# Kernel optimization log

Measured on AMD Instinct MI355X. Metric: run time of the kernel, lower is better.

Reference implementation:

```python
import jax, jax.numpy as jnp
import numpy as np

B, N, DIN, D, HID, C, K = 16, 1024, 768, 512, 128, 20, 64
H = W = 32
EPS = 1e-5  # BatchNorm eps (inference mode with running stats)


def _conv(x, w, pad=0, dil=1):
    return jax.lax.conv_general_dilated(
        x, w, (1, 1), [(pad, pad), (pad, pad)],
        rhs_dilation=(dil, dil),
        dimension_numbers=('NCHW', 'OIHW', 'NCHW'))


def _bn(x, g, b, m, v):
    inv = jax.lax.rsqrt(v + EPS)
    return (x - m[None, :, None, None]) * (g * inv)[None, :, None, None] + b[None, :, None, None]


def _l2norm(x):
    n = jnp.sqrt(jnp.sum(x * x, axis=-1, keepdims=True))
    return x / jnp.maximum(n, 1e-12)  # matches F.normalize(eps=1e-12)


def setup_inputs():
    key = jax.random.key(0)
    ks = jax.random.split(key, 12)

    def conv_w(k, o, i, kh, kw):
        return jax.random.normal(k, (o, i, kh, kw), jnp.float32) / np.sqrt(i * kh * kw)

    def bn_p(k, c):
        k1, k2 = jax.random.split(k)
        return (jnp.ones(c, jnp.float32), jnp.zeros(c, jnp.float32),
                0.1 * jax.random.normal(k1, (c,), jnp.float32),
                jax.random.uniform(k2, (c,), jnp.float32, 0.5, 1.5))

    g0, b0, m0, v0 = bn_p(ks[3], D)
    gr, br, mr, vr = bn_p(ks[4], HID)
    gl, bl, ml, vl = bn_p(ks[5], HID)
    gg, bg, mg, vg = bn_p(ks[6], HID)
    gp, bp, mp, vp = bn_p(ks[7], D)
    return {
        'patch_feats': jax.random.normal(ks[0], (B, N, DIN), jnp.float32),
        'protos': _l2norm(jax.random.normal(ks[1], (C, K, D), jnp.float32)),  # hybrid protos, L2-normed as in __init__
        'w0': conv_w(ks[2], D, DIN, 1, 1), 'g0': g0, 'b0': b0, 'm0': m0, 'v0': v0,
        'wr': conv_w(ks[8], HID, D, 1, 1), 'gr': gr, 'br': br, 'mr': mr, 'vr': vr,
        'wl': conv_w(ks[9], HID, HID, 3, 3), 'gl': gl, 'bl': bl, 'ml': ml, 'vl': vl,
        'wg': conv_w(ks[10], HID, HID, 3, 3), 'gg': gg, 'bg': bg, 'mg': mg, 'vg': vg,
        'wp': conv_w(ks[11], D, 2 * HID, 1, 1), 'gp': gp, 'bp': bp, 'mp': mp, 'vp': vp,
        'wf': conv_w(jax.random.fold_in(key, 99), D, D, 1, 1),
        'bf': jnp.zeros(D, jnp.float32),
        'logit_scale': jnp.float32(10.0),
    }


def reference(patch_feats, protos, w0, g0, b0, m0, v0, wr, gr, br, mr, vr,
              wl, gl, bl, ml, vl, wg, gg, bg, mg, vg, wp, gp, bp, mp, vp,
              wf, bf, logit_scale):
    Bq, Nq, Din = patch_feats.shape
    x = patch_feats.transpose(0, 2, 1).reshape(Bq, Din, H, W)
    # adapter: 1x1 conv -> BN -> ReLU
    x = jax.nn.relu(_bn(_conv(x, w0), g0, b0, m0, v0))
    # ResidualContextBlock
    res = x
    o = jax.nn.relu(_bn(_conv(x, wr), gr, br, mr, vr))
    l = jax.nn.relu(_bn(_conv(o, wl, pad=1), gl, bl, ml, vl))
    g = jax.nn.relu(_bn(_conv(o, wg, pad=2, dil=2), gg, bg, mg, vg))
    o = _bn(_conv(jnp.concatenate([l, g], axis=1), wp), gp, bp, mp, vp)
    x = jax.nn.relu(o + res)
    # final 1x1 conv (with bias)
    x = _conv(x, wf) + bf[None, :, None, None]
    # back to [B, N, D], L2 normalize
    x = x.reshape(Bq, D, Nq).transpose(0, 2, 1)
    x = _l2norm(x)
    # per-class cosine sims + double max reduction (vectorized over classes)
    sims = jnp.einsum('bnd,ckd->bcnk', x, protos)  # [B,C,N,K]
    A = sims.max(axis=-1)                          # [B,C,N] patch->proto max
    act_maps = A.reshape(Bq, C, H, W)
    logits = A.max(axis=-1) * logit_scale          # [B,C]
    return logits, act_maps, x
```

## Files before the change

### kernel.cpp

```cpp
#include <hip/hip_runtime.h>
#include <math.h>

#define BN_EPS 1e-5f

typedef __attribute__((ext_vector_type(8))) short short8v;
typedef __attribute__((ext_vector_type(8))) unsigned short ushort8v;
typedef __attribute__((ext_vector_type(4))) float f32x4;

__device__ __forceinline__ unsigned short f2b(float f) {
    unsigned int u = __float_as_uint(f);
    return (unsigned short)((u + 0x7FFFu + ((u >> 16) & 1u)) >> 16);
}
__device__ __forceinline__ float b2f(unsigned short h) {
    return __uint_as_float(((unsigned int)h) << 16);
}

typedef __attribute__((address_space(1))) const unsigned int gas_uint;
typedef __attribute__((address_space(3))) unsigned int las_uint;
__device__ __forceinline__ void gload16(const void* g, void* l) {
    __builtin_amdgcn_global_load_lds((gas_uint*)g, (las_uint*)l, 16, 0, 0);
}

__global__ __launch_bounds__(256) void f2b_kernel(
    const float* __restrict__ in, unsigned short* __restrict__ out, int n8)
{
    int i = blockIdx.x * 256 + threadIdx.x;
    if (i >= n8) return;
    const float4* p = (const float4*)(in + (size_t)i * 8);
    float4 a = p[0], b = p[1];
    ushort8v r;
    r[0] = f2b(a.x); r[1] = f2b(a.y); r[2] = f2b(a.z); r[3] = f2b(a.w);
    r[4] = f2b(b.x); r[5] = f2b(b.y); r[6] = f2b(b.z); r[7] = f2b(b.w);
    *(ushort8v*)(out + (size_t)i * 8) = r;
}

__global__ __launch_bounds__(256) void f2b_multi(
    const float* __restrict__ w0, const float* __restrict__ wr,
    const float* __restrict__ wp, const float* __restrict__ wf,
    const float* __restrict__ prot,
    unsigned short* __restrict__ w0o, unsigned short* __restrict__ wro,
    unsigned short* __restrict__ wpo, unsigned short* __restrict__ wfo,
    unsigned short* __restrict__ proto)
{
    int i = blockIdx.x * 256 + threadIdx.x;
    const float* src; unsigned short* dst; int off;
    if      (i <  49152) { src = w0;   dst = w0o;   off = i; }
    else if (i <  57344) { src = wr;   dst = wro;   off = i - 49152; }
    else if (i <  73728) { src = wp;   dst = wpo;   off = i - 57344; }
    else if (i < 106496) { src = wf;   dst = wfo;   off = i - 73728; }
    else if (i < 188416) { src = prot; dst = proto; off = i - 106496; }
    else return;
    const float4* p = (const float4*)(src + (size_t)off * 8);
    float4 a = p[0], b = p[1];
    ushort8v r;
    r[0] = f2b(a.x); r[1] = f2b(a.y); r[2] = f2b(a.z); r[3] = f2b(a.w);
    r[4] = f2b(b.x); r[5] = f2b(b.y); r[6] = f2b(b.z); r[7] = f2b(b.w);
    *(ushort8v*)(dst + (size_t)off * 8) = r;
}

__global__ __launch_bounds__(256) void convw_kernel(
    const float* __restrict__ wl, const float* __restrict__ wg,
    unsigned short* __restrict__ out)
{
    int i = blockIdx.x * 256 + threadIdx.x;
    if (i >= 294912) return;
    int br = i >= 147456;
    int j  = i - br * 147456;
    int tap = j >> 14, oc = (j >> 7) & 127, ic = j & 127;
    const float* src = br ? wg : wl;
    out[i] = f2b(src[((oc << 7) + ic) * 9 + tap]);
}

__global__ __launch_bounds__(256) void zero_kernel(unsigned short* __restrict__ p, int n8)
{
    int i = blockIdx.x * 256 + threadIdx.x;
    if (i >= n8) return;
    ushort8v z;
#pragma unroll
    for (int k = 0; k < 8; ++k) z[k] = 0;
    *(ushort8v*)(p + (size_t)i * 8) = z;
}

template <int EPI>
__global__ __launch_bounds__(256, 3) void mfma_gemm(
    const unsigned short* __restrict__ A, int lda,
    const unsigned short* __restrict__ Wt, int ldw,
    void* __restrict__ outp, int ldc, int Kdim,
    const float* __restrict__ bng, const float* __restrict__ bnb,
    const float* __restrict__ bnm, const float* __restrict__ bnv,
    const unsigned short* __restrict__ res, int ldres,
    const float* __restrict__ bias)
{
    __shared__ short8v Asta[2][512];
    __shared__ short8v Bsta[2][512];
    const int t  = threadIdx.x;
    const int l  = t & 63, wv = t >> 6;
    const int wm = wv >> 1, wn = wv & 1;
    const int m0 = blockIdx.x << 7, n0 = blockIdx.y << 7;

    const int r0  = t & 127;
    const int kb0 = t >> 7;

    const unsigned short* Ap = A  + (size_t)(m0 + r0) * lda + kb0 * 8;
    const unsigned short* Bp = Wt + (size_t)(n0 + r0) * ldw + kb0 * 8;

    f32x4 acc[4][4];
#pragma unroll
    for (int mf = 0; mf < 4; ++mf)
#pragma unroll
        for (int nf = 0; nf < 4; ++nf)
#pragma unroll
            for (int j = 0; j < 4; ++j) acc[mf][nf][j] = 0.f;

    const int arow = wm * 64 + (l & 15);
    const int brow = wn * 64 + (l & 15);
    const int kq   = l >> 4;

    const int nK = Kdim >> 5;

#define STAGE_G(buf, k0)                                     \
    do {                                                     \
        gload16(Ap + (k0),      &Asta[buf][wv * 64]);        \
        gload16(Ap + (k0) + 16, &Asta[buf][wv * 64 + 256]);  \
        gload16(Bp + (k0),      &Bsta[buf][wv * 64]);        \
        gload16(Bp + (k0) + 16, &Bsta[buf][wv * 64 + 256]);  \
    } while (0)

    STAGE_G(0, 0);
    __syncthreads();
    int cur = 0;
    for (int ks = 0; ks < nK; ++ks) {
        short8v af[4], bfv[4];
#pragma unroll
        for (int mf = 0; mf < 4; ++mf) af[mf]  = Asta[cur][kq * 128 + arow + mf * 16];
#pragma unroll
        for (int nf = 0; nf < 4; ++nf) bfv[nf] = Bsta[cur][kq * 128 + brow + nf * 16];
        if (ks + 1 < nK) STAGE_G(cur ^ 1, (ks + 1) << 5);
#pragma unroll
        for (int mf = 0; mf < 4; ++mf)
#pragma unroll
            for (int nf = 0; nf < 4; ++nf)
                acc[mf][nf] = __builtin_amdgcn_mfma_f32_16x16x32_bf16(
                    af[mf], bfv[nf], acc[mf][nf], 0, 0, 0);
        __syncthreads();
        cur ^= 1;
    }
#undef STAGE_G

    float s[4], sh[4];
    int cols[4];
#pragma unroll
    for (int nf = 0; nf < 4; ++nf) {
        int col = n0 + wn * 64 + nf * 16 + (l & 15);
        cols[nf] = col;
        if (EPI == 2) { s[nf] = 1.f; sh[nf] = bias[col]; }
        else {
            float sc = bng[col] * rsqrtf(bnv[col] + BN_EPS);
            s[nf]  = sc;
            sh[nf] = bnb[col] - bnm[col] * sc;
        }
    }
#pragma unroll
    for (int mf = 0; mf < 4; ++mf) {
#pragma unroll
        for (int j = 0; j < 4; ++j) {
            int row = m0 + wm * 64 + mf * 16 + kq * 4 + j;
#pragma unroll
            for (int nf = 0; nf < 4; ++nf) {
                float v = acc[mf][nf][j] * s[nf] + sh[nf];
                if (EPI == 1) v += b2f(res[(size_t)row * ldres + cols[nf]]);
                if (EPI != 2) v = fmaxf(v, 0.f);
                if (EPI == 2) {
                    ((float*)outp)[(size_t)row * ldc + cols[nf]] = v;
                } else if (EPI == 3) {
                    int b = row >> 10, h = (row >> 5) & 31, ww = row & 31;
                    size_t pidx = ((size_t)(b * 36 + h + 2) * 36 + (ww + 2)) * 128 + cols[nf];
                    ((unsigned short*)outp)[pidx] = f2b(v);
                } else {
                    ((unsigned short*)outp)[(size_t)row * ldc + cols[nf]] = f2b(v);
                }
            }
        }
    }
}

__global__ __launch_bounds__(256, 3) void conv_mfma(
    const unsigned short* __restrict__ opad,
    const unsigned short* __restrict__ wt_all,
    const float* __restrict__ g1, const float* __restrict__ b1,
    const float* __restrict__ m1, const float* __restrict__ v1,
    const float* __restrict__ g2, const float* __restrict__ b2,
    const float* __restrict__ m2, const float* __restrict__ v2,
    unsigned short* __restrict__ lg)
{
    __shared__ short8v Asta[2][512];
    __shared__ short8v Bsta[2][1024];
    const int t = threadIdx.x;
    const int l = t & 63, wv = t >> 6;
    const int wm = wv >> 1, wn = wv & 1;
    const int m0 = blockIdx.x << 6;
    const int br = blockIdx.y;
    const int dil = 1 + br;
    const unsigned short* wtb = wt_all + (size_t)br * 147456;

    const int r0 = t & 63;
    const int m  = m0 + r0;
    const int bb = m >> 10, h = (m >> 5) & 31, wc = m & 31;
    const ptrdiff_t pbase = ((ptrdiff_t)(bb * 36 + h + 2) * 36 + (wc + 2)) * 128;
    const unsigned short* ApT = opad + pbase + (t >> 6) * 8;
    const unsigned short* BpT = wtb + (size_t)(t & 127) * 128 + (t >> 7) * 8;

    f32x4 acc[2][4];
#pragma unroll
    for (int mf = 0; mf < 2; ++mf)
#pragma unroll
        for (int nf = 0; nf < 4; ++nf)
#pragma unroll
            for (int j = 0; j < 4; ++j) acc[mf][nf][j] = 0.f;

    const int arow = wm * 32 + (l & 15);
    const int bcol = wn * 64 + (l & 15);
    const int kq   = l >> 4;

#define STAGE_C(buf, s)                                                        \
    do {                                                                       \
        int tap_ = (s) >> 1, hh_ = ((s) & 1) * 64;                             \
        int dh_ = tap_ / 3 - 1, dw_ = tap_ % 3 - 1;                            \
        const unsigned short* Ap_ = ApT + (ptrdiff_t)((dh_ * 36 + dw_) * dil) * 128 + hh_; \
        const unsigned short* Bp_ = BpT + (size_t)tap_ * 16384 + hh_;          \
        gload16(Ap_,      &Asta[buf][wv * 64]);                                \
        gload16(Ap_ + 32, &Asta[buf][wv * 64 + 256]);                          \
        gload16(Bp_,      &Bsta[buf][wv * 64]);                                \
        gload16(Bp_ + 16, &Bsta[buf][wv * 64 + 256]);                          \
        gload16(Bp_ + 32, &Bsta[buf][wv * 64 + 512]);                          \
        gload16(Bp_ + 48, &Bsta[buf][wv * 64 + 768]);                          \
    } while (0)

    STAGE_C(0, 0);
    __syncthreads();
    int cur = 0;
    for (int s = 0; s < 18; ++s) {
        short8v af[2][2], bfv[2][4];
#pragma unroll
        for (int kk = 0; kk < 2; ++kk) {
            int kb = kk * 4 + kq;
            af[kk][0] = Asta[cur][kb * 64 + arow];
            af[kk][1] = Asta[cur][kb * 64 + arow + 16];
#pragma unroll
            for (int nf = 0; nf < 4; ++nf)
                bfv[kk][nf] = Bsta[cur][kb * 128 + bcol + nf * 16];
        }
        if (s + 1 < 18) STAGE_C(cur ^ 1, s + 1);
#pragma unroll
        for (int kk = 0; kk < 2; ++kk)
#pragma unroll
            for (int mf = 0; mf < 2; ++mf)
#pragma unroll
                for (int nf = 0; nf < 4; ++nf)
                    acc[mf][nf] = __builtin_amdgcn_mfma_f32_16x16x32_bf16(
                        af[kk][mf], bfv[kk][nf], acc[mf][nf], 0, 0, 0);
        __syncthreads();
        cur ^= 1;
    }
#undef STAGE_C

    const float* gg = br ? g2 : g1;
    const float* gb = br ? b2 : b1;
    const float* gm = br ? m2 : m1;
    const float* gv = br ? v2 : v1;
    float s4[4], sh[4];
    int cols[4];
#pragma unroll
    for (int nf = 0; nf < 4; ++nf) {
        int col = bcol + nf * 16;
        cols[nf] = col;
        float sc = gg[col] * rsqrtf(gv[col] + BN_EPS);
        s4[nf] = sc;
        sh[nf] = gb[col] - gm[col] * sc;
    }
#pragma unroll
    for (int mf = 0; mf < 2; ++mf) {
#pragma unroll
        for (int j = 0; j < 4; ++j) {
            int row = m0 + wm * 32 + mf * 16 + kq * 4 + j;
#pragma unroll
            for (int nf = 0; nf < 4; ++nf) {
                float v = fmaxf(acc[mf][nf][j] * s4[nf] + sh[nf], 0.f);
                lg[(size_t)row * 256 + br * 128 + cols[nf]] = f2b(v);
            }
        }
    }
}

__global__ __launch_bounds__(256) void l2norm_rows(
    float* __restrict__ x, unsigned short* __restrict__ xn)
{
    const int t    = threadIdx.x;
    const int wv   = t >> 6, lane = t & 63;
    const int row  = (blockIdx.x << 2) + wv;
    float* p = x + (size_t)row * 512 + (lane << 3);
    float4 a = *(float4*)p;
    float4 b = *(float4*)(p + 4);
    float ss = a.x * a.x + a.y * a.y + a.z * a.z + a.w * a.w +
               b.x * b.x + b.y * b.y + b.z * b.z + b.w * b.w;
#pragma unroll
    for (int off = 32; off >= 1; off >>= 1) ss += __shfl_xor(ss, off);
    float sc = 1.f / fmaxf(sqrtf(ss), 1e-12f);
    a.x *= sc; a.y *= sc; a.z *= sc; a.w *= sc;
    b.x *= sc; b.y *= sc; b.z *= sc; b.w *= sc;
    *(float4*)p       = a;
    *(float4*)(p + 4) = b;
    ushort8v r;
    r[0] = f2b(a.x); r[1] = f2b(a.y); r[2] = f2b(a.z); r[3] = f2b(a.w);
    r[4] = f2b(b.x); r[5] = f2b(b.y); r[6] = f2b(b.z); r[7] = f2b(b.w);
    *(ushort8v*)(xn + (size_t)row * 512 + (lane << 3)) = r;
}

__global__ __launch_bounds__(256, 3) void sims_mfma(
    const unsigned short* __restrict__ xn,
    const unsigned short* __restrict__ protos,
    float* __restrict__ act)
{
    __shared__ short8v Asta[2][512];
    __shared__ short8v Bsta[2][512];
    const int t = threadIdx.x;
    const int l = t & 63, wv = t >> 6;
    const int wm = wv >> 1, wn = wv & 1;
    const int m0 = blockIdx.x << 7;

    const int r0  = t & 127, kb0 = t >> 7;
    const unsigned short* Ap = xn + (size_t)(m0 + r0) * 512 + kb0 * 8;
    const unsigned short* Bp = protos + ((size_t)blockIdx.y * 128 + r0) * 512 + kb0 * 8;

    f32x4 acc[4][4];
#pragma unroll
    for (int mf = 0; mf < 4; ++mf)
#pragma unroll
        for (int nf = 0; nf < 4; ++nf)
#pragma unroll
            for (int j = 0; j < 4; ++j) acc[mf][nf][j] = 0.f;

    const int arow = wm * 64 + (l & 15);
    const int brow = wn * 64 + (l & 15);
    const int kq   = l >> 4;

#define STAGE_S(buf, k0)                                     \
    do {                                                     \
        gload16(Ap + (k0),      &Asta[buf][wv * 64]);        \
        gload16(Ap + (k0) + 16, &Asta[buf][wv * 64 + 256]);  \
        gload16(Bp + (k0),      &Bsta[buf][wv * 64]);        \
        gload16(Bp + (k0) + 16, &Bsta[buf][wv * 64 + 256]);  \
    } while (0)

    STAGE_S(0, 0);
    __syncthreads();
    int cur = 0;
    for (int ks = 0; ks < 16; ++ks) {
        short8v af[4], bfv[4];
#pragma unroll
        for (int mf = 0; mf < 4; ++mf) af[mf]  = Asta[cur][kq * 128 + arow + mf * 16];
#pragma unroll
        for (int nf = 0; nf < 4; ++nf) bfv[nf] = Bsta[cur][kq * 128 + brow + nf * 16];
        if (ks + 1 < 16) STAGE_S(cur ^ 1, (ks + 1) << 5);
#pragma unroll
        for (int mf = 0; mf < 4; ++mf)
#pragma unroll
            for (int nf = 0; nf < 4; ++nf)
                acc[mf][nf] = __builtin_amdgcn_mfma_f32_16x16x32_bf16(
                    af[mf], bfv[nf], acc[mf][nf], 0, 0, 0);
        __syncthreads();
        cur ^= 1;
    }
#undef STAGE_S

    const int c = (blockIdx.y << 1) + wn;
#pragma unroll
    for (int mf = 0; mf < 4; ++mf) {
        float vj[4];
#pragma unroll
        for (int j = 0; j < 4; ++j) {
            float v = fmaxf(fmaxf(acc[mf][0][j], acc[mf][1][j]),
                            fmaxf(acc[mf][2][j], acc[mf][3][j]));
            v = fmaxf(v, __shfl_xor(v, 1));
            v = fmaxf(v, __shfl_xor(v, 2));
            v = fmaxf(v, __shfl_xor(v, 4));
            v = fmaxf(v, __shfl_xor(v, 8));
            vj[j] = v;
        }
        if ((l & 15) == 0) {
            int rowb = m0 + wm * 64 + mf * 16 + kq * 4;
#pragma unroll
            for (int j = 0; j < 4; ++j) {
                int row = rowb + j;
                int bb = row >> 10, n = row & 1023;
                act[(((size_t)(bb * 20 + c)) << 10) + n] = vj[j];
            }
        }
    }
}

__global__ __launch_bounds__(256) void logits_max(
    const float* __restrict__ act, const float* __restrict__ lsc,
    float* __restrict__ logits)
{
    const int bc = blockIdx.x;
    const int t  = threadIdx.x;
    float4 v = *(const float4*)(act + ((size_t)bc << 10) + (t << 2));
    float mx = fmaxf(fmaxf(v.x, v.y), fmaxf(v.z, v.w));
#pragma unroll
    for (int off = 32; off >= 1; off >>= 1) mx = fmaxf(mx, __shfl_xor(mx, off));
    __shared__ float wmred[4];
    if ((t & 63) == 0) wmred[t >> 6] = mx;
    __syncthreads();
    if (t == 0) {
        float m2 = fmaxf(fmaxf(wmred[0], wmred[1]), fmaxf(wmred[2], wmred[3]));
        logits[bc] = m2 * lsc[0];
    }
}

extern "C" void kernel_launch(void* const* d_in, const int* in_sizes, int n_in,
                              void* d_out, int out_size, void* d_ws, size_t ws_size,
                              hipStream_t stream)
{
    const float* pf   = (const float*)d_in[0];
    const float* prot = (const float*)d_in[1];
    const float* w0   = (const float*)d_in[2];
    const float* g0   = (const float*)d_in[3];
    const float* b0   = (const float*)d_in[4];
    const float* m0v  = (const float*)d_in[5];
    const float* v0   = (const float*)d_in[6];
    const float* wr   = (const float*)d_in[7];
    const float* gr   = (const float*)d_in[8];
    const float* br   = (const float*)d_in[9];
    const float* mr   = (const float*)d_in[10];
    const float* vr   = (const float*)d_in[11];
    const float* wl   = (const float*)d_in[12];
    const float* gl   = (const float*)d_in[13];
    const float* bl   = (const float*)d_in[14];
    const float* ml   = (const float*)d_in[15];
    const float* vl   = (const float*)d_in[16];
    const float* wg   = (const float*)d_in[17];
    const float* gG   = (const float*)d_in[18];
    const float* bG   = (const float*)d_in[19];
    const float* mG   = (const float*)d_in[20];
    const float* vG   = (const float*)d_in[21];
    const float* wp   = (const float*)d_in[22];
    const float* gp   = (const float*)d_in[23];
    const float* bp   = (const float*)d_in[24];
    const float* mp   = (const float*)d_in[25];
    const float* vp   = (const float*)d_in[26];
    const float* wf   = (const float*)d_in[27];
    const float* bf_  = (const float*)d_in[28];
    const float* lsc  = (const float*)d_in[29];

    char* ws = (char*)d_ws;
    unsigned short* pf_bf    = (unsigned short*)(ws);
    unsigned short* w0_bf    = (unsigned short*)(ws + 25165824);
    unsigned short* wr_bf    = (unsigned short*)(ws + 25952256);
    unsigned short* wt_bf    = (unsigned short*)(ws + 26083328);
    unsigned short* wp_bf    = (unsigned short*)(ws + 26673152);
    unsigned short* wf_bf    = (unsigned short*)(ws + 26935296);
    unsigned short* prot_bf  = (unsigned short*)(ws + 27459584);
    unsigned short* x1_bf    = (unsigned short*)(ws + 28770304);
    unsigned short* opad     = (unsigned short*)(ws + 45547520);
    unsigned short* lg_bf    = (unsigned short*)(ws + 50855936);
    unsigned short* x2_bf    = (unsigned short*)(ws + 59244544);
    unsigned short* xn_bf    = (unsigned short*)(ws + 76021760);

    float* out    = (float*)d_out;
    float* logits = out;
    float* act    = out + 320;
    float* xo     = out + 328000;

    f2b_kernel<<<6144, 256, 0, stream>>>(pf, pf_bf, 1572864);
    f2b_multi<<<736, 256, 0, stream>>>(w0, wr, wp, wf, prot,
                                       w0_bf, wr_bf, wp_bf, wf_bf, prot_bf);
    convw_kernel<<<1152, 256, 0, stream>>>(wl, wg, wt_bf);
    zero_kernel<<<1296, 256, 0, stream>>>(opad, 331776);

    mfma_gemm<0><<<dim3(128, 4), 256, 0, stream>>>(
        pf_bf, 768, w0_bf, 768, x1_bf, 512, 768,
        g0, b0, m0v, v0, nullptr, 0, nullptr);

    mfma_gemm<3><<<dim3(128, 1), 256, 0, stream>>>(
        x1_bf, 512, wr_bf, 512, opad, 0, 512,
        gr, br, mr, vr, nullptr, 0, nullptr);

    conv_mfma<<<dim3(256, 2), 256, 0, stream>>>(
        opad, wt_bf, gl, bl, ml, vl, gG, bG, mG, vG, lg_bf);

    mfma_gemm<1><<<dim3(128, 4), 256, 0, stream>>>(
        lg_bf, 256, wp_bf, 256, x2_bf, 512, 256,
        gp, bp, mp, vp, x1_bf, 512, nullptr);

    mfma_gemm<2><<<dim3(128, 4), 256, 0, stream>>>(
        x2_bf, 512, wf_bf, 512, xo, 512, 512,
        nullptr, nullptr, nullptr, nullptr, nullptr, 0, bf_);

    l2norm_rows<<<4096, 256, 0, stream>>>(xo, xn_bf);

    sims_mfma<<<dim3(128, 10), 256, 0, stream>>>(xn_bf, prot_bf, act);

    logits_max<<<320, 256, 0, stream>>>(act, lsc, logits);
}
```

Measured before the change: 198.0 us.

## Deepen K-tile to 64, issue prefetch before LDS reads, add explicit waits and setprio

The GEMM and sims kernels now stage a 64-wide K slice per iteration instead of 32, doubling LDS buffers and halving the number of barrier round-trips. In all three MFMA loops the next-stage global-to-LDS prefetch is issued before the LDS fragment reads. __syncthreads is replaced by explicit vmcnt/lgkmcnt waits, a sched barrier and s_barrier, and s_setprio raises wave priority around the MFMA block. The intent is to hide global latency and cut sync overhead. The larger LDS footprint (64 KB per block) may reduce occupancy under the 3-block launch bound.

Result: slower. 209.5 us (+5.8%).

```diff
diff --git a/kernel.cpp b/kernel.cpp
--- a/kernel.cpp
+++ b/kernel.cpp
@@ -20,6 +20,11 @@
 __device__ __forceinline__ void gload16(const void* g, void* l) {
     __builtin_amdgcn_global_load_lds((gas_uint*)g, (las_uint*)l, 16, 0, 0);
 }
+
+#define VMCNT0()  asm volatile("s_waitcnt vmcnt(0)"  ::: "memory")
+#define LGKM0()   asm volatile("s_waitcnt lgkmcnt(0)" ::: "memory")
+#define SBAR()    __builtin_amdgcn_s_barrier()
+#define SCHED0()  __builtin_amdgcn_sched_barrier(0)
 
 __global__ __launch_bounds__(256) void f2b_kernel(
     const float* __restrict__ in, unsigned short* __restrict__ out, int n8)
@@ -91,18 +96,15 @@
     const unsigned short* __restrict__ res, int ldres,
     const float* __restrict__ bias)
 {
-    __shared__ short8v Asta[2][512];
-    __shared__ short8v Bsta[2][512];
+    __shared__ short8v Asta[2][1024];
+    __shared__ short8v Bsta[2][1024];
     const int t  = threadIdx.x;
     const int l  = t & 63, wv = t >> 6;
     const int wm = wv >> 1, wn = wv & 1;
     const int m0 = blockIdx.x << 7, n0 = blockIdx.y << 7;
 
-    const int r0  = t & 127;
-    const int kb0 = t >> 7;
-
-    const unsigned short* Ap = A  + (size_t)(m0 + r0) * lda + kb0 * 8;
-    const unsigned short* Bp = Wt + (size_t)(n0 + r0) * ldw + kb0 * 8;
+    const unsigned short* Ap = A  + (size_t)(m0 + (t & 127)) * lda + (t >> 7) * 8;
+    const unsigned short* Bp = Wt + (size_t)(n0 + (t & 127)) * ldw + (t >> 7) * 8;
 
     f32x4 acc[4][4];
 #pragma unroll
@@ -115,34 +117,43 @@
     const int arow = wm * 64 + (l & 15);
     const int brow = wn * 64 + (l & 15);
     const int kq   = l >> 4;
-
-    const int nK = Kdim >> 5;
-
-#define STAGE_G(buf, k0)                                     \
-    do {                                                     \
-        gload16(Ap + (k0),      &Asta[buf][wv * 64]);        \
-        gload16(Ap + (k0) + 16, &Asta[buf][wv * 64 + 256]);  \
-        gload16(Bp + (k0),      &Bsta[buf][wv * 64]);        \
-        gload16(Bp + (k0) + 16, &Bsta[buf][wv * 64 + 256]);  \
+    const int nK   = Kdim >> 6;
+
+#define STAGE_G(buf, k0)                                                   \
+    do {                                                                   \
+        _Pragma("unroll")                                                  \
+        for (int i_ = 0; i_ < 4; ++i_) {                                   \
+            gload16(Ap + (k0) + 16 * i_, &Asta[buf][wv * 64 + 256 * i_]);  \
+            gload16(Bp + (k0) + 16 * i_, &Bsta[buf][wv * 64 + 256 * i_]);  \
+        }                                                                  \
     } while (0)
 
     STAGE_G(0, 0);
-    __syncthreads();
+    VMCNT0(); SBAR();
     int cur = 0;
     for (int ks = 0; ks < nK; ++ks) {
-        short8v af[4], bfv[4];
-#pragma unroll
-        for (int mf = 0; mf < 4; ++mf) af[mf]  = Asta[cur][kq * 128 + arow + mf * 16];
-#pragma unroll
-        for (int nf = 0; nf < 4; ++nf) bfv[nf] = Bsta[cur][kq * 128 + brow + nf * 16];
-        if (ks + 1 < nK) STAGE_G(cur ^ 1, (ks + 1) << 5);
-#pragma unroll
-        for (int mf = 0; mf < 4; ++mf)
-#pragma unroll
-            for (int nf = 0; nf < 4; ++nf)
-                acc[mf][nf] = __builtin_amdgcn_mfma_f32_16x16x32_bf16(
-                    af[mf], bfv[nf], acc[mf][nf], 0, 0, 0);
-        __syncthreads();
+        if (ks + 1 < nK) STAGE_G(cur ^ 1, (ks + 1) << 6);
+        short8v af[2][4], bfv[2][4];
+#pragma unroll
+        for (int kk = 0; kk < 2; ++kk) {
+            int kb = kq + 4 * kk;
+#pragma unroll
+            for (int mf = 0; mf < 4; ++mf) af[kk][mf]  = Asta[cur][kb * 128 + arow + mf * 16];
+#pragma unroll
+            for (int nf = 0; nf < 4; ++nf) bfv[kk][nf] = Bsta[cur][kb * 128 + brow + nf * 16];
+        }
+        LGKM0(); SCHED0();
+        __builtin_amdgcn_s_setprio(1);
+#pragma unroll
+        for (int kk = 0; kk < 2; ++kk)
+#pragma unroll
+            for (int mf = 0; mf < 4; ++mf)
+#pragma unroll
+                for (int nf = 0; nf < 4; ++nf)
+                    acc[mf][nf] = __builtin_amdgcn_mfma_f32_16x16x32_bf16(
+                        af[kk][mf], bfv[kk][nf], acc[mf][nf], 0, 0, 0);
+        __builtin_amdgcn_s_setprio(0);
+        VMCNT0(); SBAR();
         cur ^= 1;
     }
 #undef STAGE_G
@@ -237,9 +248,10 @@
     } while (0)
 
     STAGE_C(0, 0);
-    __syncthreads();
+    VMCNT0(); SBAR();
     int cur = 0;
     for (int s = 0; s < 18; ++s) {
+        if (s + 1 < 18) STAGE_C(cur ^ 1, s + 1);
         short8v af[2][2], bfv[2][4];
 #pragma unroll
         for (int kk = 0; kk < 2; ++kk) {
@@ -250,7 +262,8 @@
             for (int nf = 0; nf < 4; ++nf)
                 bfv[kk][nf] = Bsta[cur][kb * 128 + bcol + nf * 16];
         }
-        if (s + 1 < 18) STAGE_C(cur ^ 1, s + 1);
+        LGKM0(); SCHED0();
+        __builtin_amdgcn_s_setprio(1);
 #pragma unroll
         for (int kk = 0; kk < 2; ++kk)
 #pragma unroll
@@ -259,7 +272,8 @@
                 for (int nf = 0; nf < 4; ++nf)
                     acc[mf][nf] = __builtin_amdgcn_mfma_f32_16x16x32_bf16(
                         af[kk][mf], bfv[kk][nf], acc[mf][nf], 0, 0, 0);
-        __syncthreads();
+        __builtin_amdgcn_s_setprio(0);
+        VMCNT0(); SBAR();
         cur ^= 1;
     }
 #undef STAGE_C
@@ -321,16 +335,16 @@
     const unsigned short* __restrict__ protos,
     float* __restrict__ act)
 {
-    __shared__ short8v Asta[2][512];
-    __shared__ short8v Bsta[2][512];
+    __shared__ short8v Asta[2][1024];
+    __shared__ short8v Bsta[2][1024];
     const int t = threadIdx.x;
     const int l = t & 63, wv = t >> 6;
     const int wm = wv >> 1, wn = wv & 1;
     const int m0 = blockIdx.x << 7;
 
-    const int r0  = t & 127, kb0 = t >> 7;
-    const unsigned short* Ap = xn + (size_t)(m0 + r0) * 512 + kb0 * 8;
-    const unsigned short* Bp = protos + ((size_t)blockIdx.y * 128 + r0) * 512 + kb0 * 8;
+    const unsigned short* Ap = xn + (size_t)(m0 + (t & 127)) * 512 + (t >> 7) * 8;
+    const unsigned short* Bp = protos +
+        ((size_t)blockIdx.y * 128 + (t & 127)) * 512 + (t >> 7) * 8;
 
     f32x4 acc[4][4];
 #pragma unroll
@@ -344,31 +358,41 @@
     const int brow = wn * 64 + (l & 15);
     const int kq   = l >> 4;
 
-#define STAGE_S(buf, k0)                                     \
-    do {                                                     \
-        gload16(Ap + (k0),      &Asta[buf][wv * 64]);        \
-        gload16(Ap + (k0) + 16, &Asta[buf][wv * 64 + 256]);  \
-        gload16(Bp + (k0),      &Bsta[buf][wv * 64]);        \
-        gload16(Bp + (k0) + 16, &Bsta[buf][wv * 64 + 256]);  \
+#define STAGE_S(buf, k0)                                                   \
+    do {                                                                   \
+        _Pragma("unroll")                                                  \
+        for (int i_ = 0; i_ < 4; ++i_) {                                   \
+            gload16(Ap + (k0) + 16 * i_, &Asta[buf][wv * 64 + 256 * i_]);  \
+            gload16(Bp + (k0) + 16 * i_, &Bsta[buf][wv * 64 + 256 * i_]);  \
+        }                                                                  \
     } while (0)
 
     STAGE_S(0, 0);
-    __syncthreads();
+    VMCNT0(); SBAR();
     int cur = 0;
-    for (int ks = 0; ks < 16; ++ks) {
-        short8v af[4], bfv[4];
-#pragma unroll
-        for (int mf = 0; mf < 4; ++mf) af[mf]  = Asta[cur][kq * 128 + arow + mf * 16];
-#pragma unroll
-        for (int nf = 0; nf < 4; ++nf) bfv[nf] = Bsta[cur][kq * 128 + brow + nf * 16];
-        if (ks + 1 < 16) STAGE_S(cur ^ 1, (ks + 1) << 5);
-#pragma unroll
-        for (int mf = 0; mf < 4; ++mf)
-#pragma unroll
-            for (int nf = 0; nf < 4; ++nf)
-                acc[mf][nf] = __builtin_amdgcn_mfma_f32_16x16x32_bf16(
-                    af[mf], bfv[nf], acc[mf][nf], 0, 0, 0);
-        __syncthreads();
+    for (int ks = 0; ks < 8; ++ks) {
+        if (ks + 1 < 8) STAGE_S(cur ^ 1, (ks + 1) << 6);
+        short8v af[2][4], bfv[2][4];
+#pragma unroll
+        for (int kk = 0; kk < 2; ++kk) {
+            int kb = kq + 4 * kk;
+#pragma unroll
+            for (int mf = 0; mf < 4; ++mf) af[kk][mf]  = Asta[cur][kb * 128 + arow + mf * 16];
+#pragma unroll
+            for (int nf = 0; nf < 4; ++nf) bfv[kk][nf] = Bsta[cur][kb * 128 + brow + nf * 16];
+        }
+        LGKM0(); SCHED0();
+        __builtin_amdgcn_s_setprio(1);
+#pragma unroll
+        for (int kk = 0; kk < 2; ++kk)
+#pragma unroll
+            for (int mf = 0; mf < 4; ++mf)
+#pragma unroll
+                for (int nf = 0; nf < 4; ++nf)
+                    acc[mf][nf] = __builtin_amdgcn_mfma_f32_16x16x32_bf16(
+                        af[kk][mf], bfv[kk][nf], acc[mf][nf], 0, 0, 0);
+        __builtin_amdgcn_s_setprio(0);
+        VMCNT0(); SBAR();
         cur ^= 1;
     }
 #undef STAGE_S
```
